# Performance work log

Hardware: AMD Instinct MI355X
Metric: run time of the kernel (lower is better)

The kernel has to match this reference:

```python
import jax, jax.numpy as jnp
import numpy as np

V, D, H, O = 50257, 256, 256, 10
L, N = 2048, 64


def setup_inputs() -> dict:
    key = jax.random.key(0)
    ks = jax.random.split(key, 20)
    s = 0.05
    p = {
        'x': jax.random.randint(ks[0], (L, N), 0, V, dtype=jnp.int64) if jax.config.jax_enable_x64 else jax.random.randint(ks[0], (L, N), 0, V, dtype=jnp.int32),
        'emb': jax.random.normal(ks[1], (V, D), jnp.float32) * s,
        'Wii': jax.random.normal(ks[2], (H, D), jnp.float32) * s, 'bii': jnp.zeros((H,), jnp.float32),
        'Whi': jax.random.normal(ks[3], (H, H), jnp.float32) * s, 'bhi': jnp.zeros((H,), jnp.float32),
        'Wif': jax.random.normal(ks[4], (H, D), jnp.float32) * s, 'bif': jnp.zeros((H,), jnp.float32),
        'Whf': jax.random.normal(ks[5], (H, H), jnp.float32) * s, 'bhf': jnp.zeros((H,), jnp.float32),
        'Wig': jax.random.normal(ks[6], (H, D), jnp.float32) * s, 'big': jnp.zeros((H,), jnp.float32),
        'Whg': jax.random.normal(ks[7], (H, H), jnp.float32) * s, 'bhg': jnp.zeros((H,), jnp.float32),
        'Wio': jax.random.normal(ks[8], (H, D), jnp.float32) * s, 'bio': jnp.zeros((H,), jnp.float32),
        'Who': jax.random.normal(ks[9], (H, H), jnp.float32) * s, 'bho': jnp.zeros((H,), jnp.float32),
        'Wout': jax.random.normal(ks[10], (O, H), jnp.float32) * s, 'bout': jnp.zeros((O,), jnp.float32),
    }
    return p


def _lstm_last_h(xe, Wii, bii, Whi, bhi, Wif, bif, Whf, bhf,
                 Wig, big, Whg, bhg, Wio, bio, Who, bho):
    # xe: [L, N, D]. Precompute all input-side gate projections in one big GEMM-like pass.
    xi = jnp.einsum('lnd,hd->lnh', xe, Wii) + bii
    xf = jnp.einsum('lnd,hd->lnh', xe, Wif) + bif
    xg = jnp.einsum('lnd,hd->lnh', xe, Wig) + big
    xo = jnp.einsum('lnd,hd->lnh', xe, Wio) + bio

    n = xe.shape[1]
    h0 = jnp.zeros((n, Whi.shape[0]), xe.dtype)
    c0 = jnp.zeros((n, Whi.shape[0]), xe.dtype)

    def step(carry, gates):
        h, c = carry
        gi, gf, gg, go = gates
        it = jax.nn.sigmoid(gi + h @ Whi.T + bhi)
        ft = jax.nn.sigmoid(gf + h @ Whf.T + bhf)
        gt = jnp.tanh(gg + h @ Whg.T + bhg)
        ot = jax.nn.sigmoid(go + h @ Who.T + bho)
        ct = ft * c + it * gt
        ht = ot * jnp.tanh(ct)
        return (ht, ct), None

    (hT, _), _ = jax.lax.scan(step, (h0, c0), (xi, xf, xg, xo))
    return hT  # [N, H]


def reference(x, emb, Wii, bii, Whi, bhi, Wif, bif, Whf, bhf,
              Wig, big, Whg, bhg, Wio, bio, Who, bho, Wout, bout):
    # EmbeddingBag with bag size 1 and mode='mean' == plain embedding lookup
    xe = emb[x]  # [L, N, D]
    hT = _lstm_last_h(xe, Wii, bii, Whi, bhi, Wif, bif, Whf, bhf,
                      Wig, big, Whg, bhg, Wio, bio, Who, bho)
    return hT @ Wout.T + bout  # [N, O]
```

## Files before the change

kernel.cpp:

```cpp
#include <hip/hip_runtime.h>


using half_t  = _Float16;
using half2_t = __attribute__((ext_vector_type(2))) _Float16;
using half8_t = __attribute__((ext_vector_type(8))) _Float16;
using f32x4   = __attribute__((ext_vector_type(4))) float;

#define L_SEQ   2048
#define CHUNK_L 1024
#define NB      64
#define DIM     256
#define P4      1024
#define CM      (CHUNK_L * NB)

#define OFF_GATES 0ull
#define SZ_GATES  ((unsigned long long)CM * P4 * 2)
#define OFF_EMBH  (OFF_GATES + SZ_GATES)
#define SZ_EMBH   (50257ull * 256 * 2)
#define OFF_WX    (OFF_EMBH + SZ_EMBH)
#define SZ_WX     (1024ull * 256 * 2)
#define OFF_WH    (OFF_WX + SZ_WX)
#define SZ_WH     (1024ull * 256 * 2)
#define OFF_B4    (OFF_WH + SZ_WH)
#define SZ_B4     (1024ull * 4)
#define OFF_ST    (OFF_B4 + SZ_B4)
#define SZ_ST     (2ull * NB * DIM * 4)
#define WS_NEED   (OFF_ST + SZ_ST)

__device__ __forceinline__ float sigm(float x) {
  x = fminf(fmaxf(x, -30.f), 30.f);
  return 1.f / (1.f + __expf(-x));
}
__device__ __forceinline__ float tanh_(float x) {
  x = fminf(fmaxf(x, -15.f), 15.f);
  float t = __expf(2.f * x);
  return (t - 1.f) / (t + 1.f);
}
__device__ __forceinline__ float dot8(half8_t w, half8_t h, float acc) {
  acc = __builtin_amdgcn_fdot2((half2_t)__builtin_shufflevector(w, w, 0, 1),
                               (half2_t)__builtin_shufflevector(h, h, 0, 1), acc, false);
  acc = __builtin_amdgcn_fdot2((half2_t)__builtin_shufflevector(w, w, 2, 3),
                               (half2_t)__builtin_shufflevector(h, h, 2, 3), acc, false);
  acc = __builtin_amdgcn_fdot2((half2_t)__builtin_shufflevector(w, w, 4, 5),
                               (half2_t)__builtin_shufflevector(h, h, 4, 5), acc, false);
  acc = __builtin_amdgcn_fdot2((half2_t)__builtin_shufflevector(w, w, 6, 7),
                               (half2_t)__builtin_shufflevector(h, h, 6, 7), acc, false);
  return acc;
}

__global__ void ws_too_small_kernel(float* out, float sz) {
  if (threadIdx.x == 0 && blockIdx.x == 0) out[0] = sz;
}

__global__ void cvt_emb_kernel(const float* __restrict__ src, half_t* __restrict__ dst,
                               int total8) {
  int i = blockIdx.x * blockDim.x + threadIdx.x;
  if (i >= total8) return;
  const float4* s = (const float4*)src + (size_t)i * 2;
  float4 a = s[0], b = s[1];
  half8_t o;
  o[0] = (half_t)a.x; o[1] = (half_t)a.y; o[2] = (half_t)a.z; o[3] = (half_t)a.w;
  o[4] = (half_t)b.x; o[5] = (half_t)b.y; o[6] = (half_t)b.z; o[7] = (half_t)b.w;
  *((half8_t*)dst + i) = o;
}

__global__ void pack_w_kernel(const float* __restrict__ Wii, const float* __restrict__ Whi,
                              const float* __restrict__ Wif, const float* __restrict__ Whf,
                              const float* __restrict__ Wig, const float* __restrict__ Whg,
                              const float* __restrict__ Wio, const float* __restrict__ Who,
                              const float* __restrict__ bii, const float* __restrict__ bhi,
                              const float* __restrict__ bif, const float* __restrict__ bhf,
                              const float* __restrict__ big_, const float* __restrict__ bhg,
                              const float* __restrict__ bio, const float* __restrict__ bho,
                              half_t* __restrict__ Wx4h, half_t* __restrict__ Wh4c,
                              float* __restrict__ b4) {
  int p = blockIdx.x;
  int k = threadIdx.x;
  int g = p >> 8, h = p & 255;
  const float* Wx = g == 0 ? Wii : g == 1 ? Wif : g == 2 ? Wig : Wio;
  const float* Wh = g == 0 ? Whi : g == 1 ? Whf : g == 2 ? Whg : Who;
  Wx4h[(size_t)p * DIM + k] = (half_t)Wx[h * DIM + k];
  Wh4c[((size_t)(k >> 3) * P4 + p) * 8 + (k & 7)] = (half_t)Wh[h * DIM + k];
  if (k == 0) {
    const float* bx = g == 0 ? bii : g == 1 ? bif : g == 2 ? big_ : bio;
    const float* bh = g == 0 ? bhi : g == 1 ? bhf : g == 2 ? bhg : bho;
    b4[p] = bx[h] + bh[h];
  }
}

#define BK   32
#define LSTR 40
__global__ __launch_bounds__(256) void gemm_gates_kernel(
    const half_t* __restrict__ embh, const int* __restrict__ xc,
    const half_t* __restrict__ Wx4h, const float* __restrict__ b4,
    half_t* __restrict__ gates) {
  __shared__ __align__(16) half_t As[128 * LSTR];
  __shared__ __align__(16) half_t Ws[128 * LSTR];
  const int tid  = threadIdx.x;
  const int lane = tid & 63;
  const int wave = tid >> 6;
  const int wm = wave >> 1, wn = wave & 1;
  const int M0 = blockIdx.x * 128;
  const int P0 = blockIdx.y * 128;
  const int r0 = tid >> 2, s0 = tid & 3;

  const size_t arow0 = (size_t)xc[M0 + r0] * DIM;
  const size_t arow1 = (size_t)xc[M0 + 64 + r0] * DIM;
  const size_t wrow0 = (size_t)(P0 + r0) * DIM;
  const size_t wrow1 = (size_t)(P0 + 64 + r0) * DIM;

  f32x4 acc[4][4] = {};
  const int fr = lane & 15;
  const int kq = lane >> 4;

  for (int kt = 0; kt < 8; ++kt) {
    const int k0 = kt * BK;
    half8_t a0 = *(const half8_t*)(embh + arow0 + k0 + s0 * 8);
    half8_t a1 = *(const half8_t*)(embh + arow1 + k0 + s0 * 8);
    half8_t w0 = *(const half8_t*)(Wx4h + wrow0 + k0 + s0 * 8);
    half8_t w1 = *(const half8_t*)(Wx4h + wrow1 + k0 + s0 * 8);
    __syncthreads();
    *(half8_t*)(As + r0 * LSTR + s0 * 8)        = a0;
    *(half8_t*)(As + (r0 + 64) * LSTR + s0 * 8) = a1;
    *(half8_t*)(Ws + r0 * LSTR + s0 * 8)        = w0;
    *(half8_t*)(Ws + (r0 + 64) * LSTR + s0 * 8) = w1;
    __syncthreads();
    half8_t af[4], bf[4];
#pragma unroll
    for (int mi = 0; mi < 4; ++mi)
      af[mi] = *(const half8_t*)(As + (wm * 64 + mi * 16 + fr) * LSTR + kq * 8);
#pragma unroll
    for (int ni = 0; ni < 4; ++ni)
      bf[ni] = *(const half8_t*)(Ws + (wn * 64 + ni * 16 + fr) * LSTR + kq * 8);
#pragma unroll
    for (int mi = 0; mi < 4; ++mi)
#pragma unroll
      for (int ni = 0; ni < 4; ++ni)
        acc[mi][ni] = __builtin_amdgcn_mfma_f32_16x16x32_f16(af[mi], bf[ni], acc[mi][ni], 0, 0, 0);
  }
  const int rbase = (lane >> 4) * 4;
#pragma unroll
  for (int ni = 0; ni < 4; ++ni) {
    const int p = P0 + wn * 64 + ni * 16 + fr;
    const float bias = b4[p];
#pragma unroll
    for (int mi = 0; mi < 4; ++mi) {
      const int m = M0 + wm * 64 + mi * 16 + rbase;
#pragma unroll
      for (int r = 0; r < 4; ++r)
        gates[(size_t)(m + r) * P4 + p] = (half_t)(acc[mi][ni][r] + bias);
    }
  }
}

#define DECL_W(i) half8_t W_##i##_0, W_##i##_1, W_##i##_2, W_##i##_3;
#define LOAD_W(i)                           \
  W_##i##_0 = W8[(kc0 + i) * P4 + b0];      \
  W_##i##_1 = W8[(kc0 + i) * P4 + b1];      \
  W_##i##_2 = W8[(kc0 + i) * P4 + b2];      \
  W_##i##_3 = W8[(kc0 + i) * P4 + b3];
#define PIN_W(i)                                                            \
  asm volatile("" : "+v"(W_##i##_0), "+v"(W_##i##_1), "+v"(W_##i##_2),      \
                    "+v"(W_##i##_3));
#define DOT_W(i) {                          \
    const half8_t h8 = hp[i];               \
    a0 = dot8(W_##i##_0, h8, a0);           \
    a1 = dot8(W_##i##_1, h8, a1);           \
    a2 = dot8(W_##i##_2, h8, a2);           \
    a3 = dot8(W_##i##_3, h8, a3); }

__global__ __launch_bounds__(512)
__attribute__((amdgpu_num_vgpr(256)))
void lstm_kernel(
    const half_t* __restrict__ gates, const half_t* __restrict__ Wh4c,
    const float* __restrict__ Wout, const float* __restrict__ bout,
    float* __restrict__ out, float* __restrict__ state,
    int first, int last) {
  const int n   = blockIdx.x;
  const int tid = threadIdx.x;
  const int j   = tid & 255;
  const int kh  = tid >> 8;
  __shared__ __align__(16) half_t wlds[8][P4][8];
  __shared__ __align__(16) half_t hbuf[2][DIM];
  __shared__ __align__(16) float  partial4[DIM][4];
  __shared__ float hfin[DIM];

  const half8_t* W8 = (const half8_t*)Wh4c;
  for (int i = tid; i < 8192; i += 512) {
    const int slot = i >> 10, p = i & 1023;
    const int kc = (slot >> 2) * 16 + 12 + (slot & 3);
    *(half8_t*)wlds[slot][p] = W8[kc * P4 + p];
  }
  const int kc0 = kh * 16;
  const int b0 = j, b1 = 256 + j, b2 = 512 + j, b3 = 768 + j;

  DECL_W(0) DECL_W(1) DECL_W(2) DECL_W(3) DECL_W(4) DECL_W(5)
  DECL_W(6) DECL_W(7) DECL_W(8) DECL_W(9) DECL_W(10) DECL_W(11)
  LOAD_W(0) LOAD_W(1) LOAD_W(2) LOAD_W(3) LOAD_W(4) LOAD_W(5)
  LOAD_W(6) LOAD_W(7) LOAD_W(8) LOAD_W(9) LOAD_W(10) LOAD_W(11)
  PIN_W(0) PIN_W(1) PIN_W(2) PIN_W(3) PIN_W(4) PIN_W(5)
  PIN_W(6) PIN_W(7) PIN_W(8) PIN_W(9) PIN_W(10) PIN_W(11)

  float c = 0.f, hkeep = 0.f;
  if (kh == 0) {
    float h0 = 0.f;
    if (!first) { h0 = state[n * DIM + j]; c = state[NB * DIM + n * DIM + j]; }
    hbuf[0][j] = (half_t)h0;
    hkeep = h0;
  }
  const half_t* gbase = gates + (size_t)n * P4;
  float g0 = 0.f, g1 = 0.f, g2 = 0.f, g3 = 0.f;
  if (kh == 1) {
    g0 = (float)gbase[b0]; g1 = (float)gbase[b1];
    g2 = (float)gbase[b2]; g3 = (float)gbase[b3];
  }
  __syncthreads();

#pragma unroll 1
  for (int l = 0; l < CHUNK_L; ++l) {
    float a0 = 0.f, a1 = 0.f, a2 = 0.f, a3 = 0.f;
    half_t ng0 = (half_t)0.f, ng1 = ng0, ng2 = ng0, ng3 = ng0;
    if (kh == 1) {
      a0 = g0; a1 = g1; a2 = g2; a3 = g3;
      const half_t* gp2 = gbase + (size_t)(l + 1) * NB * P4;
      ng0 = gp2[b0]; ng1 = gp2[b1]; ng2 = gp2[b2]; ng3 = gp2[b3];
    }
    const half8_t* hp = (const half8_t*)hbuf[l & 1] + kc0;
    DOT_W(0) DOT_W(1) DOT_W(2) DOT_W(3)
    DOT_W(4) DOT_W(5) DOT_W(6) DOT_W(7)
    DOT_W(8) DOT_W(9) DOT_W(10) DOT_W(11)
#pragma unroll
    for (int s = 0; s < 4; ++s) {
      const half8_t h8 = hp[12 + s];
      const int slot = kh * 4 + s;
      a0 = dot8(*(const half8_t*)wlds[slot][b0], h8, a0);
      a1 = dot8(*(const half8_t*)wlds[slot][b1], h8, a1);
      a2 = dot8(*(const half8_t*)wlds[slot][b2], h8, a2);
      a3 = dot8(*(const half8_t*)wlds[slot][b3], h8, a3);
    }
    if (kh == 1) {
      float4 pv; pv.x = a0; pv.y = a1; pv.z = a2; pv.w = a3;
      *(float4*)partial4[j] = pv;
      g0 = (float)ng0; g1 = (float)ng1; g2 = (float)ng2; g3 = (float)ng3;
    }
    __syncthreads();
    if (kh == 0) {
      float4 pv = *(const float4*)partial4[j];
      a0 += pv.x; a1 += pv.y; a2 += pv.z; a3 += pv.w;
      const float it = sigm(a0), ft = sigm(a1), gt = tanh_(a2), ot = sigm(a3);
      c = ft * c + it * gt;
      const float h = ot * tanh_(c);
      hbuf[(l + 1) & 1][j] = (half_t)h;
      hkeep = h;
    }
    __syncthreads();
  }
  if (kh == 0) {
    if (!last) { state[n * DIM + j] = hkeep; state[NB * DIM + n * DIM + j] = c; }
    hfin[j] = hkeep;
  }
  __syncthreads();
  if (last && tid < 10) {
    float s = bout[tid];
    const float* wrow = Wout + tid * DIM;
#pragma unroll 4
    for (int k = 0; k < DIM; ++k) s += hfin[k] * wrow[k];
    out[n * 10 + tid] = s;
  }
}

extern "C" void kernel_launch(void* const* d_in, const int* in_sizes, int n_in,
                              void* d_out, int out_size, void* d_ws, size_t ws_size,
                              hipStream_t stream) {
  const int*   x    = (const int*)d_in[0];
  const float* emb  = (const float*)d_in[1];
  const float* Wii  = (const float*)d_in[2];  const float* bii = (const float*)d_in[3];
  const float* Whi  = (const float*)d_in[4];  const float* bhi = (const float*)d_in[5];
  const float* Wif  = (const float*)d_in[6];  const float* bif = (const float*)d_in[7];
  const float* Whf  = (const float*)d_in[8];  const float* bhf = (const float*)d_in[9];
  const float* Wig  = (const float*)d_in[10]; const float* big_ = (const float*)d_in[11];
  const float* Whg  = (const float*)d_in[12]; const float* bhg = (const float*)d_in[13];
  const float* Wio  = (const float*)d_in[14]; const float* bio = (const float*)d_in[15];
  const float* Who  = (const float*)d_in[16]; const float* bho = (const float*)d_in[17];
  const float* Wout = (const float*)d_in[18]; const float* bout = (const float*)d_in[19];
  float* out = (float*)d_out;

  if (ws_size < WS_NEED) {
    hipLaunchKernelGGL(ws_too_small_kernel, dim3(1), dim3(64), 0, stream, out, (float)ws_size);
    return;
  }
  char* ws = (char*)d_ws;
  half_t* gates = (half_t*)(ws + OFF_GATES);
  half_t* embh  = (half_t*)(ws + OFF_EMBH);
  half_t* Wx4h  = (half_t*)(ws + OFF_WX);
  half_t* Wh4c  = (half_t*)(ws + OFF_WH);
  float*  b4    = (float*)(ws + OFF_B4);
  float*  state = (float*)(ws + OFF_ST);

  const int total8 = 50257 * 32;
  hipLaunchKernelGGL(cvt_emb_kernel, dim3((total8 + 255) / 256), dim3(256), 0, stream,
                     emb, embh, total8);
  hipLaunchKernelGGL(pack_w_kernel, dim3(1024), dim3(256), 0, stream,
                     Wii, Whi, Wif, Whf, Wig, Whg, Wio, Who,
                     bii, bhi, bif, bhf, big_, bhg, bio, bho,
                     Wx4h, Wh4c, b4);
  hipLaunchKernelGGL(gemm_gates_kernel, dim3(CM / 128, P4 / 128), dim3(256), 0, stream,
                     embh, x, Wx4h, b4, gates);
  hipLaunchKernelGGL(lstm_kernel, dim3(NB), dim3(512), 0, stream,
                     gates, Wh4c, Wout, bout, out, state, 1, 0);
  hipLaunchKernelGGL(gemm_gates_kernel, dim3(CM / 128, P4 / 128), dim3(256), 0, stream,
                     embh, x + (size_t)CHUNK_L * NB, Wx4h, b4, gates);
  hipLaunchKernelGGL(lstm_kernel, dim3(NB), dim3(512), 0, stream,
                     gates, Wh4c, Wout, bout, out, state, 0, 1);
}
```

Before: 3.430 ms.

## Split recurrent K dimension across four thread groups and drop LDS weight tiles

```diff
diff --git a/kernel.cpp b/kernel.cpp
--- a/kernel.cpp
+++ b/kernel.cpp
@@ -169,8 +169,7 @@
     a2 = dot8(W_##i##_2, h8, a2);           \
     a3 = dot8(W_##i##_3, h8, a3); }
 
-__global__ __launch_bounds__(512)
-__attribute__((amdgpu_num_vgpr(256)))
+__global__ __launch_bounds__(1024)
 void lstm_kernel(
     const half_t* __restrict__ gates, const half_t* __restrict__ Wh4c,
     const float* __restrict__ Wout, const float* __restrict__ bout,
@@ -180,26 +179,20 @@
   const int tid = threadIdx.x;
   const int j   = tid & 255;
   const int kh  = tid >> 8;
-  __shared__ __align__(16) half_t wlds[8][P4][8];
   __shared__ __align__(16) half_t hbuf[2][DIM];
-  __shared__ __align__(16) float  partial4[DIM][4];
+  __shared__ __align__(16) float  partial4[3][DIM][4];
   __shared__ float hfin[DIM];
 
   const half8_t* W8 = (const half8_t*)Wh4c;
-  for (int i = tid; i < 8192; i += 512) {
-    const int slot = i >> 10, p = i & 1023;
-    const int kc = (slot >> 2) * 16 + 12 + (slot & 3);
-    *(half8_t*)wlds[slot][p] = W8[kc * P4 + p];
-  }
-  const int kc0 = kh * 16;
+  const int kc0 = kh * 8;
   const int b0 = j, b1 = 256 + j, b2 = 512 + j, b3 = 768 + j;
 
-  DECL_W(0) DECL_W(1) DECL_W(2) DECL_W(3) DECL_W(4) DECL_W(5)
-  DECL_W(6) DECL_W(7) DECL_W(8) DECL_W(9) DECL_W(10) DECL_W(11)
-  LOAD_W(0) LOAD_W(1) LOAD_W(2) LOAD_W(3) LOAD_W(4) LOAD_W(5)
-  LOAD_W(6) LOAD_W(7) LOAD_W(8) LOAD_W(9) LOAD_W(10) LOAD_W(11)
-  PIN_W(0) PIN_W(1) PIN_W(2) PIN_W(3) PIN_W(4) PIN_W(5)
-  PIN_W(6) PIN_W(7) PIN_W(8) PIN_W(9) PIN_W(10) PIN_W(11)
+  DECL_W(0) DECL_W(1) DECL_W(2) DECL_W(3)
+  DECL_W(4) DECL_W(5) DECL_W(6) DECL_W(7)
+  LOAD_W(0) LOAD_W(1) LOAD_W(2) LOAD_W(3)
+  LOAD_W(4) LOAD_W(5) LOAD_W(6) LOAD_W(7)
+  PIN_W(0) PIN_W(1) PIN_W(2) PIN_W(3)
+  PIN_W(4) PIN_W(5) PIN_W(6) PIN_W(7)
 
   float c = 0.f, hkeep = 0.f;
   if (kh == 0) {
@@ -210,7 +203,7 @@
   }
   const half_t* gbase = gates + (size_t)n * P4;
   float g0 = 0.f, g1 = 0.f, g2 = 0.f, g3 = 0.f;
-  if (kh == 1) {
+  if (kh == 0) {
     g0 = (float)gbase[b0]; g1 = (float)gbase[b1];
     g2 = (float)gbase[b2]; g3 = (float)gbase[b3];
   }
@@ -220,7 +213,7 @@
   for (int l = 0; l < CHUNK_L; ++l) {
     float a0 = 0.f, a1 = 0.f, a2 = 0.f, a3 = 0.f;
     half_t ng0 = (half_t)0.f, ng1 = ng0, ng2 = ng0, ng3 = ng0;
-    if (kh == 1) {
+    if (kh == 0) {
       a0 = g0; a1 = g1; a2 = g2; a3 = g3;
       const half_t* gp2 = gbase + (size_t)(l + 1) * NB * P4;
       ng0 = gp2[b0]; ng1 = gp2[b1]; ng2 = gp2[b2]; ng3 = gp2[b3];
@@ -228,30 +221,25 @@
     const half8_t* hp = (const half8_t*)hbuf[l & 1] + kc0;
     DOT_W(0) DOT_W(1) DOT_W(2) DOT_W(3)
     DOT_W(4) DOT_W(5) DOT_W(6) DOT_W(7)
-    DOT_W(8) DOT_W(9) DOT_W(10) DOT_W(11)
-#pragma unroll
-    for (int s = 0; s < 4; ++s) {
-      const half8_t h8 = hp[12 + s];
-      const int slot = kh * 4 + s;
-      a0 = dot8(*(const half8_t*)wlds[slot][b0], h8, a0);
-      a1 = dot8(*(const half8_t*)wlds[slot][b1], h8, a1);
-      a2 = dot8(*(const half8_t*)wlds[slot][b2], h8, a2);
-      a3 = dot8(*(const half8_t*)wlds[slot][b3], h8, a3);
-    }
-    if (kh == 1) {
+    if (kh != 0) {
       float4 pv; pv.x = a0; pv.y = a1; pv.z = a2; pv.w = a3;
-      *(float4*)partial4[j] = pv;
-      g0 = (float)ng0; g1 = (float)ng1; g2 = (float)ng2; g3 = (float)ng3;
+      *(float4*)partial4[kh - 1][j] = pv;
     }
     __syncthreads();
     if (kh == 0) {
-      float4 pv = *(const float4*)partial4[j];
-      a0 += pv.x; a1 += pv.y; a2 += pv.z; a3 += pv.w;
+      float4 p1 = *(const float4*)partial4[0][j];
+      float4 p2 = *(const float4*)partial4[1][j];
+      float4 p3 = *(const float4*)partial4[2][j];
+      a0 += p1.x + p2.x + p3.x;
+      a1 += p1.y + p2.y + p3.y;
+      a2 += p1.z + p2.z + p3.z;
+      a3 += p1.w + p2.w + p3.w;
       const float it = sigm(a0), ft = sigm(a1), gt = tanh_(a2), ot = sigm(a3);
       c = ft * c + it * gt;
       const float h = ot * tanh_(c);
       hbuf[(l + 1) & 1][j] = (half_t)h;
       hkeep = h;
+      g0 = (float)ng0; g1 = (float)ng1; g2 = (float)ng2; g3 = (float)ng3;
     }
     __syncthreads();
   }
@@ -306,10 +294,10 @@
                      Wx4h, Wh4c, b4);
   hipLaunchKernelGGL(gemm_gates_kernel, dim3(CM / 128, P4 / 128), dim3(256), 0, stream,
                      embh, x, Wx4h, b4, gates);
-  hipLaunchKernelGGL(lstm_kernel, dim3(NB), dim3(512), 0, stream,
+  hipLaunchKernelGGL(lstm_kernel, dim3(NB), dim3(1024), 0, stream,
                      gates, Wh4c, Wout, bout, out, state, 1, 0);
   hipLaunchKernelGGL(gemm_gates_kernel, dim3(CM / 128, P4 / 128), dim3(256), 0, stream,
                      embh, x + (size_t)CHUNK_L * NB, Wx4h, b4, gates);
-  hipLaunchKernelGGL(lstm_kernel, dim3(NB), dim3(512), 0, stream,
+  hipLaunchKernelGGL(lstm_kernel, dim3(NB), dim3(1024), 0, stream,
                      gates, Wh4c, Wout, bout, out, state, 0, 1);
 }
```

After: 8.425 ms. +145.7%, slower.
